# Kernel optimization log

Hardware: AMD Instinct MI355X
Metric: run time of the kernel (lower is better)

Reference implementation:

```python
import jax, jax.numpy as jnp
import numpy as np

H = 2048  # hidden_size
I = 8192  # intermediate_size
B, S = 4, 2048


def setup_inputs() -> dict:
    key = jax.random.key(0)
    ks = jax.random.split(key, 8)
    scale = 1.0 / np.sqrt(H)
    scale_i = 1.0 / np.sqrt(I)
    x = jax.random.normal(ks[0], (B, S, H), dtype=jnp.float32)
    mask = jax.random.randint(ks[1], (B, S), 0, 2) > 0  # bool per-token routing
    # torch nn.Linear weights are [out_features, in_features]
    w1 = jax.random.normal(ks[2], (I, H), dtype=jnp.float32) * scale
    w2 = jax.random.normal(ks[3], (H, I), dtype=jnp.float32) * scale_i
    w3 = jax.random.normal(ks[4], (I, H), dtype=jnp.float32) * scale
    u1 = jax.random.normal(ks[5], (I, H), dtype=jnp.float32) * scale
    u2 = jax.random.normal(ks[6], (H, I), dtype=jnp.float32) * scale_i
    u3 = jax.random.normal(ks[7], (I, H), dtype=jnp.float32) * scale
    return {"x": x, "mask": mask, "w1": w1, "w2": w2, "w3": w3,
            "u1": u1, "u2": u2, "u3": u3}


def reference(x, mask, w1, w2, w3, u1, u2, u3):
    # branch 1 SwiGLU: silu(x @ w1^T) * (x @ w3^T), then w2
    proj1 = jax.nn.silu(jnp.einsum('bsh,ih->bsi', x, w1)) * jnp.einsum('bsh,ih->bsi', x, w3)
    proj2 = jax.nn.silu(jnp.einsum('bsh,ih->bsi', x, u1)) * jnp.einsum('bsh,ih->bsi', x, u3)
    out1 = jnp.einsum('bsi,hi->bsh', proj1, w2)
    out2 = jnp.einsum('bsi,hi->bsh', proj2, u2)
    m = mask[:, :, None]
    return jnp.where(m, out1, out2)
```

## Files before the change

kernel.cpp:

```cpp
#include <hip/hip_runtime.h>
#include <hip/hip_bf16.h>
#include <stdint.h>

#define DIM_H 2048
#define DIM_I 8192
#define TOKENS 8192
#define RB256 34
#define CROWS (RB256*256)

typedef __attribute__((ext_vector_type(8))) short bf16x8;
typedef __attribute__((ext_vector_type(4))) float f32x4;

#define MF(a,b,c) __builtin_amdgcn_mfma_f32_16x16x32_bf16((a),(b),(c),0,0,0)

__device__ __forceinline__ unsigned short f2bf(float f) {
    union { float f; unsigned u; } v; v.f = f;
    return (unsigned short)((v.u + 0x7FFF + ((v.u >> 16) & 1)) >> 16);
}

__global__ __launch_bounds__(256) void cvt_kernel(const float* __restrict__ in,
                                                  unsigned short* __restrict__ out,
                                                  int n4) {
    int stride = gridDim.x * blockDim.x;
    for (int j = blockIdx.x * blockDim.x + threadIdx.x; j < n4; j += stride) {
        float4 v = reinterpret_cast<const float4*>(in)[j];
        ushort4 o;
        o.x = f2bf(v.x); o.y = f2bf(v.y); o.z = f2bf(v.z); o.w = f2bf(v.w);
        reinterpret_cast<ushort4*>(out)[j] = o;
    }
}

__global__ __launch_bounds__(256) void cvt13_kernel(const float* __restrict__ w1,
                                                    const float* __restrict__ w3,
                                                    unsigned short* __restrict__ W13,
                                                    int n4) {
    int stride = gridDim.x * blockDim.x;
    for (int j = blockIdx.x * blockDim.x + threadIdx.x; j < n4; j += stride) {
        int flat = j << 2;
        int R = flat >> 11;
        int col = flat & 2047;
        int orow = ((R >> 4) << 5) | (R & 15);
        float4 v1 = reinterpret_cast<const float4*>(w1)[j];
        float4 v3 = reinterpret_cast<const float4*>(w3)[j];
        ushort4 o1, o3;
        o1.x=f2bf(v1.x); o1.y=f2bf(v1.y); o1.z=f2bf(v1.z); o1.w=f2bf(v1.w);
        o3.x=f2bf(v3.x); o3.y=f2bf(v3.y); o3.z=f2bf(v3.z); o3.w=f2bf(v3.w);
        *reinterpret_cast<ushort4*>(&W13[(size_t)orow * DIM_H + col]) = o1;
        *reinterpret_cast<ushort4*>(&W13[(size_t)(orow + 16) * DIM_H + col]) = o3;
    }
}

__global__ __launch_bounds__(256) void compact_kernel(const int* __restrict__ mask,
                                                      int* __restrict__ idx,
                                                      int* __restrict__ hdr) {
    __shared__ int cnt[256];
    const int t = threadIdx.x;
    const int base = t * 32;
    unsigned bits = 0;
#pragma unroll
    for (int j = 0; j < 32; ++j)
        if (mask[base + j] != 0) bits |= (1u << j);
    const int c = __popc(bits);
    cnt[t] = c;
    __syncthreads();
    for (int off = 1; off < 256; off <<= 1) {
        int v = cnt[t];
        int add = (t >= off) ? cnt[t - off] : 0;
        __syncthreads();
        cnt[t] = v + add;
        __syncthreads();
    }
    const int Mw  = cnt[255];
    const int MwP = (Mw + 255) & ~255;
    const int Mu  = TOKENS - Mw;
    const int MuP = (Mu + 255) & ~255;

    for (int j = t; j < CROWS; j += 256) idx[j] = -1;
    __syncthreads();

    int pw = cnt[t] - c;
    int pz = base - pw;
#pragma unroll
    for (int j = 0; j < 32; ++j) {
        int tok = base + j;
        if ((bits >> j) & 1) idx[pw++] = tok;
        else                 idx[MwP + pz++] = tok;
    }
    if (t == 0) {
        hdr[0] = MwP >> 8;
        hdr[1] = (MwP + MuP) >> 8;
        hdr[2] = Mw;
        hdr[3] = Mu;
    }
}


#define LDF4(D0,D1,D2,D3, SB, RB) do { \
    const unsigned short* _sl = &smem[(SB)]; \
    D0 = *reinterpret_cast<const bf16x8*>(&_sl[((RB) +  0)*32 + c16r]); \
    D1 = *reinterpret_cast<const bf16x8*>(&_sl[((RB) + 16)*32 + c16r]); \
    D2 = *reinterpret_cast<const bf16x8*>(&_sl[((RB) + 32)*32 + c16r]); \
    D3 = *reinterpret_cast<const bf16x8*>(&_sl[((RB) + 48)*32 + c16r]); \
} while(0)

#define STAGE2(UB_, S0_, S1_, KOFS_) do { \
    __builtin_amdgcn_global_load_lds((const __attribute__((address_space(1))) void*)((S0_) + (KOFS_)), \
        (__attribute__((address_space(3))) void*)&smem[(UB_) + wave*512], 16, 0, 0); \
    __builtin_amdgcn_global_load_lds((const __attribute__((address_space(1))) void*)((S1_) + (KOFS_)), \
        (__attribute__((address_space(3))) void*)&smem[(UB_) + 4096 + wave*512], 16, 0, 0); \
} while(0)

#define STAGE1(UB_, S0_, KOFS_) \
    __builtin_amdgcn_global_load_lds((const __attribute__((address_space(1))) void*)((S0_) + (KOFS_)), \
        (__attribute__((address_space(3))) void*)&smem[(UB_) + wave*512], 16, 0, 0)

#define MFMA32_G1() do { \
  acc[0][0]=MF(af0,bfr0,acc[0][0]); acc[0][1]=MF(af0,bfr1,acc[0][1]); acc[0][2]=MF(af0,bfr2,acc[0][2]); acc[0][3]=MF(af0,bfr3,acc[0][3]); \
  acc[1][0]=MF(af1,bfr0,acc[1][0]); acc[1][1]=MF(af1,bfr1,acc[1][1]); acc[1][2]=MF(af1,bfr2,acc[1][2]); acc[1][3]=MF(af1,bfr3,acc[1][3]); \
  acc[2][0]=MF(af2,bfr0,acc[2][0]); acc[2][1]=MF(af2,bfr1,acc[2][1]); acc[2][2]=MF(af2,bfr2,acc[2][2]); acc[2][3]=MF(af2,bfr3,acc[2][3]); \
  acc[3][0]=MF(af3,bfr0,acc[3][0]); acc[3][1]=MF(af3,bfr1,acc[3][1]); acc[3][2]=MF(af3,bfr2,acc[3][2]); acc[3][3]=MF(af3,bfr3,acc[3][3]); \
  acc[4][0]=MF(af4,bfr0,acc[4][0]); acc[4][1]=MF(af4,bfr1,acc[4][1]); acc[4][2]=MF(af4,bfr2,acc[4][2]); acc[4][3]=MF(af4,bfr3,acc[4][3]); \
  acc[5][0]=MF(af5,bfr0,acc[5][0]); acc[5][1]=MF(af5,bfr1,acc[5][1]); acc[5][2]=MF(af5,bfr2,acc[5][2]); acc[5][3]=MF(af5,bfr3,acc[5][3]); \
  acc[6][0]=MF(af6,bfr0,acc[6][0]); acc[6][1]=MF(af6,bfr1,acc[6][1]); acc[6][2]=MF(af6,bfr2,acc[6][2]); acc[6][3]=MF(af6,bfr3,acc[6][3]); \
  acc[7][0]=MF(af7,bfr0,acc[7][0]); acc[7][1]=MF(af7,bfr1,acc[7][1]); acc[7][2]=MF(af7,bfr2,acc[7][2]); acc[7][3]=MF(af7,bfr3,acc[7][3]); \
} while(0)

__global__ __launch_bounds__(512, 2) void gemm1_kernel(
    const unsigned short* __restrict__ xb,
    const unsigned short* __restrict__ W13,
    const unsigned short* __restrict__ U13,
    const int* __restrict__ idx, const int* __restrict__ hdr,
    unsigned short* __restrict__ P)
{
    __shared__ __align__(16) unsigned short smem[65536];
    const int wB  = hdr[0];
    const int rbT = hdr[1];
    const int nwg = gridDim.x;
    const int q8  = nwg >> 3;
    const int swzb = ((int)blockIdx.x & 7) * q8 + ((int)blockIdx.x >> 3);
    const int rb = swzb % RB256;
    const int bx = swzb / RB256;
    if (rb >= rbT) return;
    const unsigned short* Bm = (rb < wB) ? W13 : U13;
    const int bm0 = rb << 8;
    const int bn0 = bx << 8;

    const int tid  = threadIdx.x;
    const int lane = tid & 63;
    const int wave = tid >> 6;
    const int wrM = wave >> 2;
    const int wcN = wave & 3;
    const int rAb = wrM * 128 + (lane & 15);
    const int rBb = wcN * 64 + (lane & 15);
    const int c16r = (((lane >> 4) ^ ((lane >> 1) & 3))) << 3;

    const int p0 = tid, p1 = 512 + tid;
    const int r0 = p0 >> 2, r1 = p1 >> 2;
    const int c0 = ((p0 & 3) ^ ((r0 >> 1) & 3)) << 3;
    const int c1 = ((p1 & 3) ^ ((r1 >> 1) & 3)) << 3;
    int t0 = idx[bm0 + r0]; if (t0 < 0) t0 = 0;
    int t1 = idx[bm0 + r1]; if (t1 < 0) t1 = 0;
    const unsigned short* sa0 = xb + (size_t)t0 * DIM_H + c0;
    const unsigned short* sa1 = xb + (size_t)t1 * DIM_H + c1;
    const unsigned short* sb0 = Bm + (size_t)(bn0 + r0) * DIM_H + c0;
    const unsigned short* sb1 = Bm + (size_t)(bn0 + r1) * DIM_H + c1;

    f32x4 acc[8][4] = {};
    bf16x8 af0, af1, af2, af3, af4, af5, af6, af7, bfr0, bfr1, bfr2, bfr3;

    STAGE2(0,     sa0, sa1, 0);
    STAGE2(16384, sb0, sb1, 0);
    STAGE2(8192,  sa0, sa1, 32);
    STAGE2(24576, sb0, sb1, 32);
    STAGE2(32768, sa0, sa1, 64);
    STAGE2(49152, sb0, sb1, 64);
    asm volatile("s_waitcnt vmcnt(8)" ::: "memory");
    __builtin_amdgcn_s_barrier();
    int ko = 96;
    for (int t = 0; t < 32; ++t) {
        const int cur = (t & 1) << 15;
        const int nxt = cur ^ 32768;
        LDF4(af0,af1,af2,af3, cur,          rAb);
        LDF4(af4,af5,af6,af7, cur,          rAb + 64);
        LDF4(bfr0,bfr1,bfr2,bfr3, cur + 16384, rBb);
        STAGE2(nxt + 8192,  sa0, sa1, ko);
        STAGE2(nxt + 24576, sb0, sb1, ko);
        __builtin_amdgcn_s_setprio(1);
        MFMA32_G1();
        __builtin_amdgcn_s_setprio(0);
        asm volatile("s_waitcnt vmcnt(8)" ::: "memory");
        __builtin_amdgcn_s_barrier();
        LDF4(af0,af1,af2,af3, cur + 8192,   rAb);
        LDF4(af4,af5,af6,af7, cur + 8192,   rAb + 64);
        LDF4(bfr0,bfr1,bfr2,bfr3, cur + 24576, rBb);
        STAGE2(cur,         sa0, sa1, ko + 32);
        STAGE2(cur + 16384, sb0, sb1, ko + 32);
        ko += 64;
        __builtin_amdgcn_s_setprio(1);
        MFMA32_G1();
        __builtin_amdgcn_s_setprio(0);
        asm volatile("s_waitcnt vmcnt(8)" ::: "memory");
        __builtin_amdgcn_s_barrier();
    }

    const int crow = (lane >> 4) << 2;
    const int ccol = lane & 15;
    unsigned short* Pw = P + (size_t)(bm0 + wrM * 128) * DIM_I
                           + (size_t)bx * 128 + wcN * 32 + ccol;
#pragma unroll
    for (int m = 0; m < 8; ++m) {
#pragma unroll
        for (int q = 0; q < 2; ++q) {
            f32x4 h1 = acc[m][2 * q];
            f32x4 h3 = acc[m][2 * q + 1];
#pragma unroll
            for (int r = 0; r < 4; ++r) {
                float a = h1[r];
                float p = a * (1.0f / (1.0f + __expf(-a))) * h3[r];
                Pw[(size_t)(m * 16 + crow + r) * DIM_I + q * 16] = f2bf(p);
            }
        }
    }
}

#define MFMA16Q(AF0,AF1,AF2,AF3, B0,B1,B2,B3) do { \
  acc[0][0]=MF(AF0,B0,acc[0][0]); acc[0][1]=MF(AF0,B1,acc[0][1]); acc[0][2]=MF(AF0,B2,acc[0][2]); acc[0][3]=MF(AF0,B3,acc[0][3]); \
  acc[1][0]=MF(AF1,B0,acc[1][0]); acc[1][1]=MF(AF1,B1,acc[1][1]); acc[1][2]=MF(AF1,B2,acc[1][2]); acc[1][3]=MF(AF1,B3,acc[1][3]); \
  acc[2][0]=MF(AF2,B0,acc[2][0]); acc[2][1]=MF(AF2,B1,acc[2][1]); acc[2][2]=MF(AF2,B2,acc[2][2]); acc[2][3]=MF(AF2,B3,acc[2][3]); \
  acc[3][0]=MF(AF3,B0,acc[3][0]); acc[3][1]=MF(AF3,B1,acc[3][1]); acc[3][2]=MF(AF3,B2,acc[3][2]); acc[3][3]=MF(AF3,B3,acc[3][3]); \
} while(0)

__global__ __launch_bounds__(512, 2) void gemm2_kernel(
    const unsigned short* __restrict__ P,
    const unsigned short* __restrict__ w2b, const unsigned short* __restrict__ u2b,
    const int* __restrict__ idx, const int* __restrict__ hdr,
    float* __restrict__ out)
{
    __shared__ __align__(16) unsigned short smem[73728];
    const int wB2  = hdr[0] * 2;
    const int rbT2 = hdr[1] * 2;
    const int nwg = gridDim.x;
    const int q8  = nwg >> 3;
    const int swz = ((int)blockIdx.x & 7) * q8 + ((int)blockIdx.x >> 3);
    const int rb = swz % 68;
    const int bx = swz / 68;
    if (rb >= rbT2) return;
    const unsigned short* Bm = (rb < wB2) ? w2b : u2b;
    const int bm0 = rb << 7;
    const int bn0 = bx << 8;

    const int tid  = threadIdx.x;
    const int lane = tid & 63;
    const int wave = tid >> 6;
    const int wrM = wave >> 2;
    const int wcN = wave & 3;
    const int rAb = wrM * 64 + (lane & 15);
    const int rBb = wcN * 64 + (lane & 15);
    const int c16r = (((lane >> 4) ^ ((lane >> 1) & 3))) << 3;

    const int r0 = tid >> 2, r1 = 128 + r0;
    const int c0 = ((tid & 3) ^ ((r0 >> 1) & 3)) << 3;
    const int c1 = ((tid & 3) ^ ((r1 >> 1) & 3)) << 3;
    const unsigned short* sa0 = P  + (size_t)(bm0 + r0) * DIM_I + c0;
    const unsigned short* sb0 = Bm + (size_t)(bn0 + r0) * DIM_I + c0;
    const unsigned short* sb1 = Bm + (size_t)(bn0 + r1) * DIM_I + c1;

    f32x4 acc[4][4] = {};
    bf16x8 af0, af1, af2, af3, af4, af5, af6, af7;
    bf16x8 bfr0, bfr1, bfr2, bfr3, bfr4, bfr5, bfr6, bfr7;

    STAGE1(0,     sa0, 0);
    STAGE1(4096,  sa0, 32);
    STAGE2(8192,  sb0, sb1, 0);
    STAGE2(16384, sb0, sb1, 32);
    STAGE1(24576,         sa0, 64);
    STAGE1(24576 + 4096,  sa0, 96);
    STAGE2(24576 + 8192,  sb0, sb1, 64);
    STAGE2(24576 + 16384, sb0, sb1, 96);
    asm volatile("s_waitcnt vmcnt(6)" ::: "memory");
    __builtin_amdgcn_s_barrier();
    int ko = 128, cb = 0;
    for (int t = 0; t < 128; ++t) {
        const int base = cb * 24576;
        int nb = base + 49152; if (nb >= 73728) nb -= 73728;
        LDF4(af0,af1,af2,af3,     base,          rAb);
        LDF4(af4,af5,af6,af7,     base + 4096,   rAb);
        LDF4(bfr0,bfr1,bfr2,bfr3, base + 8192,   rBb);
        LDF4(bfr4,bfr5,bfr6,bfr7, base + 16384,  rBb);
        STAGE1(nb,         sa0, ko);
        STAGE1(nb + 4096,  sa0, ko + 32);
        STAGE2(nb + 8192,  sb0, sb1, ko);
        STAGE2(nb + 16384, sb0, sb1, ko + 32);
        ko += 64;
        __builtin_amdgcn_s_setprio(1);
        MFMA16Q(af0,af1,af2,af3, bfr0,bfr1,bfr2,bfr3);
        MFMA16Q(af4,af5,af6,af7, bfr4,bfr5,bfr6,bfr7);
        __builtin_amdgcn_s_setprio(0);
        asm volatile("s_waitcnt vmcnt(6)" ::: "memory");
        __builtin_amdgcn_s_barrier();
        cb = (cb == 2) ? 0 : cb + 1;
    }

    const int crow = (lane >> 4) << 2;
    const int ccol = lane & 15;
#pragma unroll
    for (int m = 0; m < 4; ++m) {
#pragma unroll
        for (int r = 0; r < 4; ++r) {
            int rowc = bm0 + wrM * 64 + m * 16 + crow + r;
            int g = idx[rowc];
            if (g >= 0) {
                float* op = out + (size_t)g * DIM_H + bn0 + wcN * 64 + ccol;
#pragma unroll
                for (int n = 0; n < 4; ++n) op[n * 16] = acc[m][n][r];
            }
        }
    }
}

extern "C" void kernel_launch(void* const* d_in, const int* in_sizes, int n_in,
                              void* d_out, int out_size, void* d_ws, size_t ws_size,
                              hipStream_t stream) {
    const float* x    = (const float*)d_in[0];
    const int*   mask = (const int*)d_in[1];
    const float* w1 = (const float*)d_in[2];
    const float* w2 = (const float*)d_in[3];
    const float* w3 = (const float*)d_in[4];
    const float* u1 = (const float*)d_in[5];
    const float* u2 = (const float*)d_in[6];
    const float* u3 = (const float*)d_in[7];
    float* out = (float*)d_out;

    const size_t XN   = (size_t)TOKENS * DIM_H;
    const size_t WN   = (size_t)DIM_I * DIM_H;
    const size_t PN   = (size_t)CROWS * DIM_I;
    const size_t W13N = 2 * WN;

    unsigned short* ws  = (unsigned short*)d_ws;
    unsigned short* xb  = ws;
    unsigned short* Pb  = xb + XN;
    unsigned short* W13 = Pb + PN;
    unsigned short* U13 = W13 + W13N;
    int* idx = (int*)(U13 + W13N);
    int* hdr = idx + CROWS;
    unsigned short* w2b = W13;
    unsigned short* u2b = U13;

    const int cvtBlocks = 2048;
    const int n4 = (int)(WN / 4);

    cvt_kernel  <<<cvtBlocks, 256, 0, stream>>>(x, xb, (int)(XN / 4));
    cvt13_kernel<<<cvtBlocks, 256, 0, stream>>>(w1, w3, W13, n4);
    cvt13_kernel<<<cvtBlocks, 256, 0, stream>>>(u1, u3, U13, n4);
    compact_kernel<<<1, 256, 0, stream>>>(mask, idx, hdr);

    gemm1_kernel<<<64 * RB256, 512, 0, stream>>>(xb, W13, U13, idx, hdr, Pb);

    cvt_kernel<<<cvtBlocks, 256, 0, stream>>>(w2, w2b, n4);
    cvt_kernel<<<cvtBlocks, 256, 0, stream>>>(u2, u2b, n4);

    gemm2_kernel<<<8 * 68, 512, 0, stream>>>(Pb, w2b, u2b, idx, hdr, out);
}
```

Baseline: 1.058 ms.

## Split gemm2 into full-wave main grid plus small-tile tail kernel

The second GEMM's 544-block grid is cut to 512 blocks covering row blocks 0-63, so the main launch fills whole waves of CUs. The remaining row blocks (64-67) go to a new tail kernel that uses 64x64 tiles with 256 threads, which spreads that work over more workgroups. This targets the wave-quantization tail of the main grid. The cost is an extra kernel launch and less efficient small tiles for the leftover rows.

```diff
diff --git a/kernel.cpp b/kernel.cpp
--- a/kernel.cpp
+++ b/kernel.cpp
@@ -101,6 +101,12 @@
     D1 = *reinterpret_cast<const bf16x8*>(&_sl[((RB) + 16)*32 + c16r]); \
     D2 = *reinterpret_cast<const bf16x8*>(&_sl[((RB) + 32)*32 + c16r]); \
     D3 = *reinterpret_cast<const bf16x8*>(&_sl[((RB) + 48)*32 + c16r]); \
+} while(0)
+
+#define LDF2(D0,D1, SB, RB) do { \
+    const unsigned short* _sl = &smem[(SB)]; \
+    D0 = *reinterpret_cast<const bf16x8*>(&_sl[((RB) +  0)*32 + c16r]); \
+    D1 = *reinterpret_cast<const bf16x8*>(&_sl[((RB) + 16)*32 + c16r]); \
 } while(0)
 
 #define STAGE2(UB_, S0_, S1_, KOFS_) do { \
@@ -242,8 +248,8 @@
     const int nwg = gridDim.x;
     const int q8  = nwg >> 3;
     const int swz = ((int)blockIdx.x & 7) * q8 + ((int)blockIdx.x >> 3);
-    const int rb = swz % 68;
-    const int bx = swz / 68;
+    const int rb = swz & 63;
+    const int bx = swz >> 6;
     if (rb >= rbT2) return;
     const unsigned short* Bm = (rb < wB2) ? w2b : u2b;
     const int bm0 = rb << 7;
@@ -318,6 +324,79 @@
     }
 }
 
+__global__ __launch_bounds__(256, 2) void gemm2_tail_kernel(
+    const unsigned short* __restrict__ P,
+    const unsigned short* __restrict__ w2b, const unsigned short* __restrict__ u2b,
+    const int* __restrict__ idx, const int* __restrict__ hdr,
+    float* __restrict__ out)
+{
+    __shared__ __align__(16) unsigned short smem[12288];
+    const int wB2  = hdr[0] * 2;
+    const int rbT2 = hdr[1] * 2;
+    const int b   = (int)blockIdx.x;
+    const int bx  = b & 31;
+    const int sub = (b >> 5) & 1;
+    const int rb  = 64 + (b >> 6);
+    if (rb >= rbT2) return;
+    const unsigned short* Bm = (rb < wB2) ? w2b : u2b;
+    const int bm0 = (rb << 7) + (sub << 6);
+    const int bn0 = bx << 6;
+
+    const int tid  = threadIdx.x;
+    const int lane = tid & 63;
+    const int wave = tid >> 6;
+    const int wrM = wave >> 1;
+    const int wcN = wave & 1;
+    const int rAb = wrM * 32 + (lane & 15);
+    const int rBb = wcN * 32 + (lane & 15);
+    const int c16r = (((lane >> 4) ^ ((lane >> 1) & 3))) << 3;
+
+    const int r0 = tid >> 2;
+    const int c0 = ((tid & 3) ^ ((r0 >> 1) & 3)) << 3;
+    const unsigned short* sa0 = P  + (size_t)(bm0 + r0) * DIM_I + c0;
+    const unsigned short* sb0 = Bm + (size_t)(bn0 + r0) * DIM_I + c0;
+
+    f32x4 acc[2][2] = {};
+    bf16x8 af0, af1, bf0, bf1;
+
+    STAGE1(0,    sa0, 0);  STAGE1(2048,        sb0, 0);
+    STAGE1(4096, sa0, 32); STAGE1(4096 + 2048, sb0, 32);
+    asm volatile("s_waitcnt vmcnt(2)" ::: "memory");
+    __builtin_amdgcn_s_barrier();
+    int ko = 64, cb = 0;
+    for (int t = 0; t < 256; ++t) {
+        const int base = cb * 4096;
+        int nb = base + 8192; if (nb >= 12288) nb -= 12288;
+        LDF2(af0,af1, base,        rAb);
+        LDF2(bf0,bf1, base + 2048, rBb);
+        STAGE1(nb, sa0, ko); STAGE1(nb + 2048, sb0, ko);
+        ko += 32;
+        __builtin_amdgcn_s_setprio(1);
+        acc[0][0]=MF(af0,bf0,acc[0][0]); acc[0][1]=MF(af0,bf1,acc[0][1]);
+        acc[1][0]=MF(af1,bf0,acc[1][0]); acc[1][1]=MF(af1,bf1,acc[1][1]);
+        __builtin_amdgcn_s_setprio(0);
+        asm volatile("s_waitcnt vmcnt(2)" ::: "memory");
+        __builtin_amdgcn_s_barrier();
+        cb = (cb == 2) ? 0 : cb + 1;
+    }
+
+    const int crow = (lane >> 4) << 2;
+    const int ccol = lane & 15;
+#pragma unroll
+    for (int m = 0; m < 2; ++m) {
+#pragma unroll
+        for (int r = 0; r < 4; ++r) {
+            int rowc = bm0 + wrM * 32 + m * 16 + crow + r;
+            int g = idx[rowc];
+            if (g >= 0) {
+                float* op = out + (size_t)g * DIM_H + bn0 + wcN * 32 + ccol;
+#pragma unroll
+                for (int n = 0; n < 2; ++n) op[n * 16] = acc[m][n][r];
+            }
+        }
+    }
+}
+
 extern "C" void kernel_launch(void* const* d_in, const int* in_sizes, int n_in,
                               void* d_out, int out_size, void* d_ws, size_t ws_size,
                               hipStream_t stream) {
@@ -359,5 +438,6 @@
     cvt_kernel<<<cvtBlocks, 256, 0, stream>>>(w2, w2b, n4);
     cvt_kernel<<<cvtBlocks, 256, 0, stream>>>(u2, u2b, n4);
 
-    gemm2_kernel<<<8 * 68, 512, 0, stream>>>(Pb, w2b, u2b, idx, hdr, out);
-}
+    gemm2_kernel<<<512, 512, 0, stream>>>(Pb, w2b, u2b, idx, hdr, out);
+    gemm2_tail_kernel<<<256, 256, 0, stream>>>(Pb, w2b, u2b, idx, hdr, out);
+}
```

Result: faster. 1.017 ms (-3.9%).
